# Optimization experiments

Measured on AMD Instinct MI355X. Metric: run time of the kernel, lower is better.

Reference implementation:

```python
import jax, jax.numpy as jnp
import numpy as np

B, T, D = 1, 2048, 2048
HQ, HKV = 32, 8
DKV = 512  # HKV * head_dim

def setup_inputs() -> dict:
    key = jax.random.key(0)
    ks = jax.random.split(key, 5)
    s = 0.02
    return {
        "x": jax.random.normal(ks[0], (B, T, D), jnp.float32),
        "q_proj": jax.random.normal(ks[1], (D, D), jnp.float32) * s,
        "k_proj": jax.random.normal(ks[2], (DKV, D), jnp.float32) * s,
        "v_proj": jax.random.normal(ks[3], (DKV, D), jnp.float32) * s,
        "o_proj": jax.random.normal(ks[4], (D, D), jnp.float32) * s,
    }

def reference(x, q_proj, k_proj, v_proj, o_proj):
    b, t, _ = x.shape
    h_q, h_kv = HQ, HKV
    q_out = x @ q_proj.T            # [b,t,D]
    k_out = x @ k_proj.T            # [b,t,DKV]
    v_out = x @ v_proj.T
    dh_q = q_out.shape[-1] // h_q   # 64
    dh_k = k_out.shape[-1] // h_kv  # 64
    q = q_out.reshape(b, t, h_q, dh_q).transpose(0, 2, 1, 3)   # [b,hq,t,dh]
    k = k_out.reshape(b, t, h_kv, dh_k).transpose(0, 2, 1, 3)  # [b,hkv,t,dh]
    v = v_out.reshape(b, t, h_kv, dh_k).transpose(0, 2, 1, 3)
    group = h_q // h_kv
    k = jnp.repeat(k, group, axis=1)  # [b,hq,t,dh]
    v = jnp.repeat(v, group, axis=1)
    attn_logits = jnp.einsum('bhqd,bhkd->bhqk', q, k) / jnp.sqrt(jnp.float32(dh_q))
    mask = jnp.tril(jnp.ones((t, t), dtype=bool))
    attn = jax.nn.softmax(jnp.where(mask, attn_logits, -1e10), axis=-1)
    ctx = jnp.einsum('bhqk,bhkd->bhqd', attn, v)
    ctx = ctx.transpose(0, 2, 1, 3).reshape(b, t, o_proj.shape[0])
    return ctx @ o_proj
```

## Files before the change

### kernel.cpp

```cpp
#include <hip/hip_runtime.h>
#include <stdint.h>

typedef __attribute__((ext_vector_type(8))) __bf16 bf16x8;
typedef __attribute__((ext_vector_type(4))) float f32x4;
typedef __attribute__((ext_vector_type(4))) unsigned short u16x4;

typedef __attribute__((address_space(1))) unsigned int as1_uint;
typedef __attribute__((address_space(3))) unsigned int as3_uint;

__device__ __forceinline__ unsigned short f2bf(float f) {
  unsigned int u = __float_as_uint(f);
  u += 0x7fffu + ((u >> 16) & 1u);
  return (unsigned short)(u >> 16);
}

__device__ __forceinline__ void gload_lds16(const void* g, void* l) {
  __builtin_amdgcn_global_load_lds((as1_uint*)(uintptr_t)g, (as3_uint*)(uintptr_t)l,
                                   16, 0, 0);
}

__global__ __launch_bounds__(256)
void cvt_fused(const float* __restrict__ x, const float* __restrict__ qp,
               const float* __restrict__ kp, const float* __restrict__ vp,
               const float* __restrict__ op,
               unsigned short* __restrict__ xb, unsigned short* __restrict__ qpb,
               unsigned short* __restrict__ kpb, unsigned short* __restrict__ vpb,
               unsigned short* __restrict__ opT) {
  __shared__ unsigned short t[64][72];
  const int b = blockIdx.x;
  if (b < 10240) {
    const float* in;
    unsigned short* out;
    int base;
    if (b < 4096)      { in = x;  out = xb;  base = b; }
    else if (b < 8192) { in = qp; out = qpb; base = b - 4096; }
    else if (b < 9216) { in = kp; out = kpb; base = b - 8192; }
    else               { in = vp; out = vpb; base = b - 9216; }
    const int i = base * 256 + threadIdx.x;
    float4 v = ((const float4*)in)[i];
    u16x4 o;
    o[0] = f2bf(v.x); o[1] = f2bf(v.y); o[2] = f2bf(v.z); o[3] = f2bf(v.w);
    ((u16x4*)out)[i] = o;
    return;
  }
  const int tb = b - 10240;
  const int tj = (tb & 31) * 64;
  const int ti = (tb >> 5) * 64;
  const int r  = threadIdx.x >> 4;
  const int c4 = (threadIdx.x & 15) * 4;
#pragma unroll
  for (int i = 0; i < 4; ++i) {
    int row = r + i * 16;
    float4 v = *(const float4*)&op[(size_t)(ti + row) * 2048 + tj + c4];
    t[row][c4]     = f2bf(v.x);
    t[row][c4 + 1] = f2bf(v.y);
    t[row][c4 + 2] = f2bf(v.z);
    t[row][c4 + 3] = f2bf(v.w);
  }
  __syncthreads();
#pragma unroll
  for (int i = 0; i < 4; ++i) {
    int orow = r + i * 16;
    u16x4 o;
    o[0] = t[c4][orow]; o[1] = t[c4 + 1][orow];
    o[2] = t[c4 + 2][orow]; o[3] = t[c4 + 3][orow];
    *(u16x4*)&opT[(size_t)(tj + orow) * 2048 + ti + c4] = o;
  }
}

template <int BN, bool OUT_BF16>
__device__ __forceinline__
void gemm_body(const unsigned short* __restrict__ A,
               const unsigned short* __restrict__ B,
               void* __restrict__ Cout, int N, int K, float alpha,
               int bx, int by, unsigned short* lA, unsigned short* lB) {
  constexpr int NF  = BN / 32;
  constexpr int ASZ = 64 * 64;
  constexpr int BSZ = BN * 64;
  const int tid  = threadIdx.x;
  const int lane = tid & 63;
  const int w    = tid >> 6;
  const int wr   = (w >> 1) * 32;
  const int wc   = (w & 1) * (BN / 2);
  const long brow = (long)by * 64;
  const long bcol = (long)bx * BN;
  const int lr = lane & 15;
  const int lq = lane >> 4;

  const int row0 = tid >> 3;
  const int lc0  = (tid & 7) ^ (row0 & 7);

  f32x4 acc[2][NF] = {};

  const unsigned short* gA = A + (brow + row0) * (long)K + lc0 * 8;
  const unsigned short* gB = B + (bcol + row0) * (long)K + lc0 * 8;

#define G_STAGE(buf, k0)                                                          \
  {                                                                               \
    gload_lds16(gA + (k0),           lA + (buf) * ASZ + tid * 8);                 \
    gload_lds16(gA + 32l * K + (k0), lA + (buf) * ASZ + 2048 + tid * 8);          \
    _Pragma("unroll")                                                             \
    for (int g = 0; g < NF; ++g)                                                  \
      gload_lds16(gB + g * 32l * K + (k0), lB + (buf) * BSZ + g * 2048 + tid * 8);\
  }

  G_STAGE(0, 0);
  __syncthreads();

  for (int k0 = 0; k0 < K; k0 += 64) {
    const int cur = (k0 >> 6) & 1;
    if (k0 + 64 < K) G_STAGE(cur ^ 1, k0 + 64);
#pragma unroll
    for (int kk = 0; kk < 2; ++kk) {
      const int j = kk * 4 + lq;
      const int ra0 = wr + lr, ra1 = wr + 16 + lr;
      bf16x8 a0 = *(const bf16x8*)&lA[cur * ASZ + ra0 * 64 + ((j ^ (ra0 & 7)) << 3)];
      bf16x8 a1 = *(const bf16x8*)&lA[cur * ASZ + ra1 * 64 + ((j ^ (ra1 & 7)) << 3)];
      bf16x8 b[NF];
#pragma unroll
      for (int n = 0; n < NF; ++n) {
        const int rb = wc + n * 16 + lr;
        b[n] = *(const bf16x8*)&lB[cur * BSZ + rb * 64 + ((j ^ (rb & 7)) << 3)];
      }
#pragma unroll
      for (int n = 0; n < NF; ++n) {
        acc[0][n] = __builtin_amdgcn_mfma_f32_16x16x32_bf16(a0, b[n], acc[0][n], 0, 0, 0);
        acc[1][n] = __builtin_amdgcn_mfma_f32_16x16x32_bf16(a1, b[n], acc[1][n], 0, 0, 0);
      }
    }
    __syncthreads();
  }
#undef G_STAGE

  const int orow = (int)brow + wr + lq * 4;
  const int ocol = (int)bcol + wc + lr;
#pragma unroll
  for (int m = 0; m < 2; ++m)
#pragma unroll
    for (int n = 0; n < NF; ++n)
#pragma unroll
      for (int r = 0; r < 4; ++r) {
        size_t row = (size_t)(orow + m * 16 + r);
        size_t col = (size_t)(ocol + n * 16);
        float v = acc[m][n][r] * alpha;
        if (OUT_BF16)
          ((unsigned short*)Cout)[row * N + col] = f2bf(v);
        else
          ((float*)Cout)[row * N + col] = v;
      }
}

template <int BN, bool OUT_BF16>
__global__ __launch_bounds__(256)
void gemm_nt(const unsigned short* __restrict__ A,
             const unsigned short* __restrict__ B,
             void* __restrict__ Cout, int N, int K, float alpha) {
  __shared__ unsigned short lA[2 * 64 * 64];
  __shared__ unsigned short lB[2 * BN * 64];
  gemm_body<BN, OUT_BF16>(A, B, Cout, N, K, alpha, blockIdx.x, blockIdx.y, lA, lB);
}

__global__ __launch_bounds__(256)
void gemm_proj(const unsigned short* __restrict__ xb,
               const unsigned short* __restrict__ qpb,
               const unsigned short* __restrict__ kpb,
               const unsigned short* __restrict__ vpb,
               unsigned short* __restrict__ Qb, unsigned short* __restrict__ Kbf,
               unsigned short* __restrict__ Vtb) {
  __shared__ unsigned short lA[2 * 64 * 64];
  __shared__ unsigned short lB[2 * 128 * 64];
  const int bid = blockIdx.x;
  const unsigned short *A, *B;
  unsigned short* C;
  int N, bx, by;
  float alpha;
  if (bid < 512) {
    A = xb;  B = qpb; C = Qb;  N = 2048; alpha = 0.125f * 1.44269504088896f;
    bx = bid & 15; by = bid >> 4;
  } else if (bid < 640) {
    int b = bid - 512;
    A = xb;  B = kpb; C = Kbf; N = 512;  alpha = 1.0f;
    bx = b & 3; by = b >> 2;
  } else {
    int b = bid - 640;
    A = vpb; B = xb;  C = Vtb; N = 2048; alpha = 1.0f;
    bx = b & 15; by = b >> 4;
  }
  gemm_body<128, true>(A, B, C, N, 2048, alpha, bx, by, lA, lB);
}

__global__ __launch_bounds__(256, 4)
void attn64(const unsigned short* __restrict__ Q,
            const unsigned short* __restrict__ Kb,
            const unsigned short* __restrict__ Vt,
            unsigned short* __restrict__ ctx) {
  constexpr int T = 2048, DQ = 2048, DKV = 512, DH = 64;
  const int h    = blockIdx.x;
  const int hkv  = h >> 2;
  const int ya   = blockIdx.y >> 3;
  const int yb   = blockIdx.y & 7;
  const int qi   = (ya == 0) ? yb : (ya == 1) ? 15 - yb : (ya == 2) ? 16 + yb : 31 - yb;
  const int tid  = threadIdx.x;
  const int lane = tid & 63;
  const int w    = tid >> 6;
  const int lr   = lane & 15;
  const int lq   = lane >> 4;
  const int lk   = lq * 8;
  const int sw   = lr & 7;

  __shared__ unsigned short lK[2][64 * 64];
  __shared__ unsigned short lV[2][64 * 64];
  __shared__ unsigned short P[4][16][64];

  const int row0 = tid >> 3;
  const int lc0  = (tid & 7) ^ (row0 & 7);

  bf16x8 ones_frag;
#pragma unroll
  for (int i = 0; i < 8; ++i) ones_frag[i] = (lr == 0) ? (__bf16)1.0f : (__bf16)0.0f;

#define STAGE_KV(bufidx, kv0)                                                        \
  {                                                                                  \
    gload_lds16(Kb + (size_t)((kv0) + row0) * DKV + hkv * DH + lc0 * 8,              \
                &lK[bufidx][tid * 8]);                                               \
    gload_lds16(Kb + (size_t)((kv0) + row0 + 32) * DKV + hkv * DH + lc0 * 8,         \
                &lK[bufidx][2048 + tid * 8]);                                        \
    gload_lds16(Vt + (size_t)(hkv * DH + row0) * T + (kv0) + lc0 * 8,                \
                &lV[bufidx][tid * 8]);                                               \
    gload_lds16(Vt + (size_t)(hkv * DH + row0 + 32) * T + (kv0) + lc0 * 8,           \
                &lV[bufidx][2048 + tid * 8]);                                        \
  }

  const int q0b = qi * 64;
  const int qw  = q0b + w * 16;

  bf16x8 qf0 = *(const bf16x8*)&Q[(size_t)(qw + lr) * DQ + h * DH + lk];
  bf16x8 qf1 = *(const bf16x8*)&Q[(size_t)(qw + lr) * DQ + h * DH + 32 + lk];

  f32x4 oacc[4] = {};
  f32x4 lacc = {};
  float mr[4];
#pragma unroll
  for (int r = 0; r < 4; ++r) mr[r] = -3.0e38f;

  const int nt = qi + 1;
  STAGE_KV(0, 0);
  __syncthreads();

  for (int t = 0; t < nt; ++t) {
    const int kv0 = t * 64;
    const int cur = t & 1;
    if (t + 1 < nt) STAGE_KV(cur ^ 1, kv0 + 64);

    f32x4 s[4];
    __builtin_amdgcn_s_setprio(1);
#pragma unroll
    for (int n = 0; n < 4; ++n) {
      const int krow = n * 16 + lr;
      bf16x8 kf0 = *(const bf16x8*)&lK[cur][krow * 64 + ((lq ^ sw) << 3)];
      bf16x8 kf1 = *(const bf16x8*)&lK[cur][krow * 64 + (((4 + lq) ^ sw) << 3)];
      f32x4 acc = {};
      acc = __builtin_amdgcn_mfma_f32_16x16x32_bf16(qf0, kf0, acc, 0, 0, 0);
      acc = __builtin_amdgcn_mfma_f32_16x16x32_bf16(qf1, kf1, acc, 0, 0, 0);
      s[n] = acc;
    }
    __builtin_amdgcn_s_setprio(0);

    if (t == qi) {
      const int qr0 = qw + (lq << 2);
#pragma unroll
      for (int n = 0; n < 4; ++n) {
        int kc = kv0 + n * 16 + lr;
#pragma unroll
        for (int r = 0; r < 4; ++r)
          if (kc > qr0 + r) s[n][r] = -3.0e38f;
      }
    }

    float lml[4];
#pragma unroll
    for (int r = 0; r < 4; ++r)
      lml[r] = fmaxf(fmaxf(s[0][r], s[1][r]), fmaxf(s[2][r], s[3][r]));
    const bool defer = __all((lml[0] <= mr[0] + 8.f) & (lml[1] <= mr[1] + 8.f) &
                             (lml[2] <= mr[2] + 8.f) & (lml[3] <= mr[3] + 8.f));
    if (!defer) {
#pragma unroll
      for (int r = 0; r < 4; ++r) {
        float ml = lml[r];
        ml = fmaxf(ml, __shfl_xor(ml, 1));
        ml = fmaxf(ml, __shfl_xor(ml, 2));
        ml = fmaxf(ml, __shfl_xor(ml, 4));
        ml = fmaxf(ml, __shfl_xor(ml, 8));
        float mnew = fmaxf(mr[r], ml);
        float sc   = __builtin_amdgcn_exp2f(mr[r] - mnew);
        mr[r] = mnew;
        lacc[r] *= sc;
        oacc[0][r] *= sc; oacc[1][r] *= sc;
        oacc[2][r] *= sc; oacc[3][r] *= sc;
      }
    }

#pragma unroll
    for (int n = 0; n < 4; ++n)
#pragma unroll
      for (int r = 0; r < 4; ++r)
        s[n][r] = __builtin_amdgcn_exp2f(s[n][r] - mr[r]);

#pragma unroll
    for (int n = 0; n < 4; ++n)
#pragma unroll
      for (int r = 0; r < 4; ++r) {
        const int prow = (lq << 2) + r;
        P[w][prow][(((2 * n + (lr >> 3)) ^ (prow & 7)) << 3) + (lr & 7)] =
            (unsigned short)(__float_as_uint(s[n][r]) >> 16);
      }
    asm volatile("s_waitcnt lgkmcnt(0)" ::: "memory");
    __builtin_amdgcn_sched_barrier(0);

    __builtin_amdgcn_s_setprio(1);
#pragma unroll
    for (int ks = 0; ks < 2; ++ks) {
      bf16x8 pf = *(const bf16x8*)&P[w][lr][((ks * 4 + lq) ^ sw) << 3];
      lacc = __builtin_amdgcn_mfma_f32_16x16x32_bf16(pf, ones_frag, lacc, 0, 0, 0);
#pragma unroll
      for (int n = 0; n < 4; ++n) {
        const int vrow = n * 16 + lr;
        bf16x8 vf = *(const bf16x8*)&lV[cur][vrow * 64 + (((ks * 4 + lq) ^ sw) << 3)];
        oacc[n] = __builtin_amdgcn_mfma_f32_16x16x32_bf16(pf, vf, oacc[n], 0, 0, 0);
      }
    }
    __builtin_amdgcn_s_setprio(0);

    __syncthreads();
  }

  float inv[4];
#pragma unroll
  for (int r = 0; r < 4; ++r) {
    float l = __shfl(lacc[r], lane & 48);
    inv[r] = 1.f / l;
  }
#pragma unroll
  for (int n = 0; n < 4; ++n)
#pragma unroll
    for (int r = 0; r < 4; ++r) {
      int qrow = qw + (lq << 2) + r;
      ctx[(size_t)qrow * DQ + h * DH + n * 16 + lr] = f2bf(oacc[n][r] * inv[r]);
    }
#undef STAGE_KV
}

extern "C" void kernel_launch(void* const* d_in, const int* in_sizes, int n_in,
                              void* d_out, int out_size, void* d_ws, size_t ws_size,
                              hipStream_t stream) {
  const float* x  = (const float*)d_in[0];
  const float* qp = (const float*)d_in[1];
  const float* kp = (const float*)d_in[2];
  const float* vp = (const float*)d_in[3];
  const float* op = (const float*)d_in[4];

  char* ws = (char*)d_ws;
  const size_t MB = 1024 * 1024;
  unsigned short* xb   = (unsigned short*)(ws + 0 * MB);
  unsigned short* qpb  = (unsigned short*)(ws + 8 * MB);
  unsigned short* kpb  = (unsigned short*)(ws + 16 * MB);
  unsigned short* vpb  = (unsigned short*)(ws + 18 * MB);
  unsigned short* opT  = (unsigned short*)(ws + 20 * MB);
  unsigned short* Qb   = (unsigned short*)(ws + 28 * MB);
  unsigned short* Kbf  = (unsigned short*)(ws + 36 * MB);
  unsigned short* Vtb  = (unsigned short*)(ws + 38 * MB);
  unsigned short* ctxb = (unsigned short*)(ws + 40 * MB);

  cvt_fused<<<11264, 256, 0, stream>>>(x, qp, kp, vp, op, xb, qpb, kpb, vpb, opT);

  gemm_proj<<<768, 256, 0, stream>>>(xb, qpb, kpb, vpb, Qb, Kbf, Vtb);

  attn64<<<dim3(32, 32), 256, 0, stream>>>(Qb, Kbf, Vtb, ctxb);

  gemm_nt<128, false><<<dim3(16, 32), 256, 0, stream>>>(ctxb, opT, d_out, 2048, 2048, 1.0f);
}
```

Measured before the change: 114.0 us.

## Shrink attention tiles to 32 queries x 32 keys with two-wave blocks

The attention kernel now processes 32-query blocks with 2 waves and 32-key KV tiles, launching twice as many blocks. K/V staging, the LDS layout of V (two head-dim rows packed per LDS row) and the shared P buffer are rewritten to fit the smaller tile. The aim is finer causal granularity, so fewer masked keys are computed, plus more blocks for occupancy and load balance. In exchange, each K/V tile is reused by fewer queries, so more global loads, barriers and loop iterations are spent per unit of work.

```diff
diff --git a/kernel.cpp b/kernel.cpp
--- a/kernel.cpp
+++ b/kernel.cpp
@@ -189,17 +189,17 @@
   gemm_body<128, true>(A, B, C, N, 2048, alpha, bx, by, lA, lB);
 }
 
-__global__ __launch_bounds__(256, 4)
-void attn64(const unsigned short* __restrict__ Q,
+__global__ __launch_bounds__(128, 4)
+void attn32(const unsigned short* __restrict__ Q,
             const unsigned short* __restrict__ Kb,
             const unsigned short* __restrict__ Vt,
             unsigned short* __restrict__ ctx) {
   constexpr int T = 2048, DQ = 2048, DKV = 512, DH = 64;
   const int h    = blockIdx.x;
   const int hkv  = h >> 2;
-  const int ya   = blockIdx.y >> 3;
-  const int yb   = blockIdx.y & 7;
-  const int qi   = (ya == 0) ? yb : (ya == 1) ? 15 - yb : (ya == 2) ? 16 + yb : 31 - yb;
+  const int ya   = blockIdx.y >> 4;
+  const int yb   = blockIdx.y & 15;
+  const int qi   = (ya == 0) ? yb : (ya == 1) ? 31 - yb : (ya == 2) ? 32 + yb : 63 - yb;
   const int tid  = threadIdx.x;
   const int lane = tid & 63;
   const int w    = tid >> 6;
@@ -208,12 +208,15 @@
   const int lk   = lq * 8;
   const int sw   = lr & 7;
 
-  __shared__ unsigned short lK[2][64 * 64];
-  __shared__ unsigned short lV[2][64 * 64];
-  __shared__ unsigned short P[4][16][64];
-
-  const int row0 = tid >> 3;
-  const int lc0  = (tid & 7) ^ (row0 & 7);
+  __shared__ unsigned short lK[2][32 * 64];
+  __shared__ unsigned short lV[2][32 * 64];
+  __shared__ unsigned short P[16][64];
+
+  const int krow0 = tid >> 3;
+  const int klc   = (tid & 7) ^ (krow0 & 7);
+  const int vlc = (tid & 7) ^ (krow0 & 7);
+  const int vdp = vlc >> 2;
+  const int vkc = vlc & 3;
 
   bf16x8 ones_frag;
 #pragma unroll
@@ -221,17 +224,18 @@
 
 #define STAGE_KV(bufidx, kv0)                                                        \
   {                                                                                  \
-    gload_lds16(Kb + (size_t)((kv0) + row0) * DKV + hkv * DH + lc0 * 8,              \
-                &lK[bufidx][tid * 8]);                                               \
-    gload_lds16(Kb + (size_t)((kv0) + row0 + 32) * DKV + hkv * DH + lc0 * 8,         \
-                &lK[bufidx][2048 + tid * 8]);                                        \
-    gload_lds16(Vt + (size_t)(hkv * DH + row0) * T + (kv0) + lc0 * 8,                \
-                &lV[bufidx][tid * 8]);                                               \
-    gload_lds16(Vt + (size_t)(hkv * DH + row0 + 32) * T + (kv0) + lc0 * 8,           \
-                &lV[bufidx][2048 + tid * 8]);                                        \
-  }
-
-  const int q0b = qi * 64;
+    _Pragma("unroll")                                                                \
+    for (int g = 0; g < 2; ++g)                                                      \
+      gload_lds16(Kb + (size_t)((kv0) + krow0 + 16 * g) * DKV + hkv * DH + klc * 8,  \
+                  &lK[bufidx][tid * 8 + g * 1024]);                                  \
+    _Pragma("unroll")                                                                \
+    for (int g = 0; g < 2; ++g)                                                      \
+      gload_lds16(Vt + (size_t)(hkv * DH + 2 * (krow0 + 16 * g) + vdp) * T +         \
+                      (kv0) + vkc * 8,                                               \
+                  &lV[bufidx][tid * 8 + g * 1024]);                                  \
+  }
+
+  const int q0b = qi * 32;
   const int qw  = q0b + w * 16;
 
   bf16x8 qf0 = *(const bf16x8*)&Q[(size_t)(qw + lr) * DQ + h * DH + lk];
@@ -248,14 +252,14 @@
   __syncthreads();
 
   for (int t = 0; t < nt; ++t) {
-    const int kv0 = t * 64;
+    const int kv0 = t * 32;
     const int cur = t & 1;
-    if (t + 1 < nt) STAGE_KV(cur ^ 1, kv0 + 64);
-
-    f32x4 s[4];
+    if (t + 1 < nt) STAGE_KV(cur ^ 1, kv0 + 32);
+
+    f32x4 s[2];
     __builtin_amdgcn_s_setprio(1);
 #pragma unroll
-    for (int n = 0; n < 4; ++n) {
+    for (int n = 0; n < 2; ++n) {
       const int krow = n * 16 + lr;
       bf16x8 kf0 = *(const bf16x8*)&lK[cur][krow * 64 + ((lq ^ sw) << 3)];
       bf16x8 kf1 = *(const bf16x8*)&lK[cur][krow * 64 + (((4 + lq) ^ sw) << 3)];
@@ -269,7 +273,7 @@
     if (t == qi) {
       const int qr0 = qw + (lq << 2);
 #pragma unroll
-      for (int n = 0; n < 4; ++n) {
+      for (int n = 0; n < 2; ++n) {
         int kc = kv0 + n * 16 + lr;
 #pragma unroll
         for (int r = 0; r < 4; ++r)
@@ -279,8 +283,7 @@
 
     float lml[4];
 #pragma unroll
-    for (int r = 0; r < 4; ++r)
-      lml[r] = fmaxf(fmaxf(s[0][r], s[1][r]), fmaxf(s[2][r], s[3][r]));
+    for (int r = 0; r < 4; ++r) lml[r] = fmaxf(s[0][r], s[1][r]);
     const bool defer = __all((lml[0] <= mr[0] + 8.f) & (lml[1] <= mr[1] + 8.f) &
                              (lml[2] <= mr[2] + 8.f) & (lml[3] <= mr[3] + 8.f));
     if (!defer) {
@@ -301,31 +304,27 @@
     }
 
 #pragma unroll
-    for (int n = 0; n < 4; ++n)
-#pragma unroll
-      for (int r = 0; r < 4; ++r)
-        s[n][r] = __builtin_amdgcn_exp2f(s[n][r] - mr[r]);
-
-#pragma unroll
-    for (int n = 0; n < 4; ++n)
+    for (int n = 0; n < 2; ++n)
 #pragma unroll
       for (int r = 0; r < 4; ++r) {
-        const int prow = (lq << 2) + r;
-        P[w][prow][(((2 * n + (lr >> 3)) ^ (prow & 7)) << 3) + (lr & 7)] =
-            (unsigned short)(__float_as_uint(s[n][r]) >> 16);
+        float p = __builtin_amdgcn_exp2f(s[n][r] - mr[r]);
+        const int prow  = (lq << 2) + r;
+        const int chunk = 4 * w + 2 * n + (lr >> 3);
+        P[prow][((chunk ^ (prow & 7)) << 3) + (lr & 7)] =
+            (unsigned short)(__float_as_uint(p) >> 16);
       }
     asm volatile("s_waitcnt lgkmcnt(0)" ::: "memory");
     __builtin_amdgcn_sched_barrier(0);
 
     __builtin_amdgcn_s_setprio(1);
-#pragma unroll
-    for (int ks = 0; ks < 2; ++ks) {
-      bf16x8 pf = *(const bf16x8*)&P[w][lr][((ks * 4 + lq) ^ sw) << 3];
+    {
+      bf16x8 pf = *(const bf16x8*)&P[lr][(((4 * w + lq) ^ sw) << 3)];
       lacc = __builtin_amdgcn_mfma_f32_16x16x32_bf16(pf, ones_frag, lacc, 0, 0, 0);
 #pragma unroll
       for (int n = 0; n < 4; ++n) {
-        const int vrow = n * 16 + lr;
-        bf16x8 vf = *(const bf16x8*)&lV[cur][vrow * 64 + (((ks * 4 + lq) ^ sw) << 3)];
+        const int vrow = 8 * n + (lr >> 1);
+        const int vch  = (((lr & 1) * 4 + lq) ^ (vrow & 7)) << 3;
+        bf16x8 vf = *(const bf16x8*)&lV[cur][vrow * 64 + vch];
         oacc[n] = __builtin_amdgcn_mfma_f32_16x16x32_bf16(pf, vf, oacc[n], 0, 0, 0);
       }
     }
@@ -375,7 +374,7 @@
 
   gemm_proj<<<768, 256, 0, stream>>>(xb, qpb, kpb, vpb, Qb, Kbf, Vtb);
 
-  attn64<<<dim3(32, 32), 256, 0, stream>>>(Qb, Kbf, Vtb, ctxb);
+  attn32<<<dim3(32, 64), 128, 0, stream>>>(Qb, Kbf, Vtb, ctxb);
 
   gemm_nt<128, false><<<dim3(16, 32), 256, 0, stream>>>(ctxb, opT, d_out, 2048, 2048, 1.0f);
 }
```

Result: slower. 124.8 us (+9.5%).
